# Kernel tuning notes

Hardware: AMD Instinct MI355X
Metric: run time of the kernel (lower is better)

Reference implementation:

```python
import jax, jax.numpy as jnp
import numpy as np
import itertools, math
from collections import Counter

# ----- circuit / state constants -----
M = 12            # modes
NPH = 5           # photons (input_state = [1]*5 + [0]*7)
NTHETA = 12       # trainable phase shifters
NX = 8            # input phase shifters (input_size)
NPARAMS = NTHETA + NX
OUT = 10
TWO_PI = 2.0 * np.pi

# all output Fock states with NPH photons in M modes, as sorted row-index multisets
ROW_IDX = np.array(list(itertools.combinations_with_replacement(range(M), NPH)), np.int32)  # [S, NPH]
S = ROW_IDX.shape[0]  # C(M+NPH-1, NPH) = 4368
# normalization prod(s_j!) for each output state (input state is 0/1 so its factor is 1)
NORM = np.array([np.prod([math.factorial(v) for v in Counter(tuple(r)).values()]) for r in ROW_IDX], np.float32)

# Ryser subsets of the NPH columns
K = 1 << NPH
MASKS = np.array([[(s >> j) & 1 for j in range(NPH)] for s in range(K)], np.float32)  # [K, NPH]
SIGNS = ((-1.0) ** (MASKS.sum(1) + NPH)).astype(np.float32)                            # [K]

# fixed 50/50 beamsplitter layers (perceval BS convention: 1/sqrt2 [[1, i],[i, 1]])
def _bs_layer(pairs):
    Bm = np.eye(M, dtype=np.complex64)
    r = np.float32(1.0 / np.sqrt(2.0))
    for (i, j) in pairs:
        Bm[i, i] = r; Bm[j, j] = r
        Bm[i, j] = 1j * r; Bm[j, i] = 1j * r
    return Bm
BS_EVEN = _bs_layer([(i, i + 1) for i in range(0, M - 1, 2)])
BS_ODD = _bs_layer([(i, i + 1) for i in range(1, M - 1, 2)])


def build_unitaries(x, thetas):
    """x: [B, NX] in [0,1]; thetas: [NTHETA]. Returns batched unitaries [B, M, M] complex64."""
    b = x.shape[0]
    phis = jnp.concatenate([jnp.broadcast_to(thetas, (b, NTHETA)), x * TWO_PI], axis=1)  # [B, NPARAMS]
    U = jnp.broadcast_to(jnp.eye(M, dtype=jnp.complex64), (b, M, M))
    for k in range(NPARAMS):
        mode = k % M
        phase = jnp.exp(1j * phis[:, k])  # [B] complex64
        ph = jnp.ones((b, M), jnp.complex64).at[:, mode].set(phase)
        U = ph[:, :, None] * U                               # apply phase shifter (diag @ U)
        Bm = jnp.asarray(BS_EVEN if k % 2 == 0 else BS_ODD)
        U = jnp.einsum('ij,bjk->bik', Bm, U)                 # apply BS layer
    return U


def slos_distribution(U):
    """Boson-sampling output distribution: p(s) = |perm(U[s_rows, :NPH])|^2 / prod(s_j!)."""
    Ucols = U[:, :, :NPH]  # photons enter modes 0..NPH-1 -> keep those columns, [B, M, NPH]
    masks = jnp.asarray(MASKS).astype(jnp.complex64)
    signs = jnp.asarray(SIGNS).astype(jnp.complex64)
    row_idx = jnp.asarray(ROW_IDX)

    def body(acc, ms):
        mask, sign = ms
        rs = Ucols @ mask              # row sums over subset columns, [B, M]
        rows = rs[:, row_idx]          # gather rows per output state, [B, S, NPH]
        return acc + sign * jnp.prod(rows, axis=-1), None

    acc0 = jnp.zeros((U.shape[0], S), jnp.complex64)
    perm, _ = jax.lax.scan(jax.checkpoint(body), acc0, (masks, signs))  # Ryser over 2^NPH subsets
    probs = (perm.real ** 2 + perm.imag ** 2) / jnp.asarray(NORM)
    return probs  # [B, S]


def setup_inputs() -> dict:
    key = jax.random.key(0)
    k1, k2, k3 = jax.random.split(key, 3)
    x = jax.random.uniform(k1, (512, NX), dtype=jnp.float32)                 # inputs in [0,1]
    thetas = jax.random.uniform(k2, (NTHETA,), dtype=jnp.float32) * np.pi    # init in [0, pi]
    W = jax.random.normal(k3, (S, OUT), dtype=jnp.float32) / np.sqrt(S)      # linear output mapping
    b = jnp.zeros((OUT,), jnp.float32)
    return {"x": x, "thetas": thetas, "W": W, "b": b}


def reference(x, thetas, W, b):
    U = build_unitaries(x, thetas)
    probs = slos_distribution(U)
    return probs @ W + b  # [B, OUT]
```

## Files before the change

### kernel.cpp

```cpp
#include <hip/hip_runtime.h>


#define MODES 12
#define NPH   5
#define KG    16
#define QG    8
#define NPAIR 78
#define S_TOT 4368
#define TPB   512
#define NWAVE (TPB / 64)
#define NOUT  10
#define NPREF 1365

#define TWO_PI_F 6.28318530717958647692f
#define RS2      0.70710678118654752440f

constexpr int Cnk(int n, int r) {
  int p = 1;
  for (int i = 0; i < r; ++i) p = p * (n - i) / (i + 1);
  return p;
}

struct Tables {
  unsigned       pref[NPREF];
  unsigned short cstart[TPB + 1];
  unsigned char  pairs[NPAIR];
};

constexpr Tables make_tables() {
  Tables T{};
  int idx = 0;
  for (int v = 11; v >= 0; --v)
    for (int m0 = 0; m0 <= v; ++m0)
      for (int m1 = m0; m1 <= v; ++m1)
        for (int m2 = m1; m2 <= v; ++m2) {
          int sbase = 0;
          for (int q = 0;  q < m0; ++q) sbase += Cnk(15 - q, 4);
          for (int q = m0; q < m1; ++q) sbase += Cnk(14 - q, 3);
          for (int q = m1; q < m2; ++q) sbase += Cnk(13 - q, 2);
          for (int q = m2; q < v;  ++q) sbase += 12 - q;
          int r1 = 1, pm = 1;
          r1 = (m1 == m0) ? r1 + 1 : 1; pm *= r1;
          r1 = (m2 == m1) ? r1 + 1 : 1; pm *= r1;
          r1 = (v  == m2) ? r1 + 1 : 1; pm *= r1;
          int code = 0;
          if (pm == 1)       code = 0;
          else if (pm == 2)  code = (r1 == 1) ? 1 : 2;
          else if (pm == 4)  code = 3;
          else if (pm == 6)  code = (r1 == 1) ? 4 : 5;
          else               code = 6;
          T.pref[idx++] = ((unsigned)code << 29) | ((unsigned)sbase << 16) |
                          ((unsigned)m0 << 12) | ((unsigned)m1 << 8) |
                          ((unsigned)m2 << 4) | (unsigned)v;
        }
  const long total = 56784;
  long cum = 0;
  int ci = 0;
  T.cstart[0] = 0;
  for (int i = 0; i < NPREF; ++i) {
    int v = (int)(T.pref[i] & 15u);
    cum += 16 + 8 * (12 - v);
    while (ci < TPB - 1 && cum * TPB >= (long)(ci + 1) * total)
      T.cstart[++ci] = (unsigned short)(i + 1);
  }
  while (ci < TPB) T.cstart[++ci] = NPREF;
  int pi = 0;
  for (int a = 0; a < MODES; ++a)
    for (int b = a; b < MODES; ++b)
      T.pairs[pi++] = (unsigned char)((a << 4) | b);
  return T;
}

__constant__ Tables g_tab = make_tables();

__constant__ float2 g_normlut[7] = {
  {1.f / 512.f,   1.f / 256.f},
  {1.f / 1024.f,  1.f / 512.f},
  {1.f / 1536.f,  1.f / 512.f},
  {1.f / 3072.f,  1.f / 1024.f},
  {1.f / 3072.f,  1.f / 1536.f},
  {1.f / 6144.f,  1.f / 1536.f},
  {1.f / 30720.f, 1.f / 6144.f},
};

#define BFLY(i, j)                                                 \
  { float ar = ur[i], ai = ui[i], br = ur[j], bi = ui[j];          \
    ur[i] = RS2 * (ar - bi); ui[i] = RS2 * (ai + br);              \
    ur[j] = RS2 * (br - ai); ui[j] = RS2 * (bi + ar); }

#define PREF(q)                                                     \
  { float4 A = ppt[q][p01], B = ppt[q][p2v];                        \
    pf##q = make_float4(A.x*B.x - A.y*B.y, A.x*B.y + A.y*B.x,       \
                        A.z*B.z - A.w*B.w, A.z*B.w + A.w*B.z); }

#define WSTEP(q, PR, PI)                                            \
  { float4 e2 = rsp[q][w];                                          \
    PR = fmaf(pf##q.x, e2.x, PR); PR = fmaf(-pf##q.y, e2.y, PR);    \
    PI = fmaf(pf##q.x, e2.y, PI); PI = fmaf(pf##q.y, e2.x, PI);     \
    PR = fmaf(pf##q.z, e2.z, PR); PR = fmaf(-pf##q.w, e2.w, PR);    \
    PI = fmaf(pf##q.z, e2.w, PI); PI = fmaf(pf##q.w, e2.z, PI); }

__global__ __launch_bounds__(TPB, 2) void qlayer_kernel(
    const float* __restrict__ x,
    const float* __restrict__ th,
    const float* __restrict__ W,
    const float* __restrict__ bias,
    float* __restrict__ out)
{
  __shared__ float4 rsp[QG][MODES];
  __shared__ float4 ppt[QG][NPAIR];
  __shared__ float  prob_lds[S_TOT];
  __shared__ float2 uc[MODES][NPH];
  __shared__ float2 sc[20];
  __shared__ float  wred[NWAVE][NOUT];

  const int b = blockIdx.x;
  const int t = threadIdx.x;

  if (t < 20) {
    float phi = (t < 12) ? th[t] : x[b * 8 + (t - 12)] * TWO_PI_F;
    float s, c;
    sincosf(phi, &s, &c);
    sc[t] = make_float2(s, c);
  }
  __syncthreads();

  if (t < NPH) {
    float ur[MODES], ui[MODES];
    #pragma unroll
    for (int m = 0; m < MODES; ++m) { ur[m] = 0.f; ui[m] = 0.f; }
    ur[t] = 1.f;
    #pragma unroll
    for (int k = 0; k < 20; ++k) {
      const int mode = k % MODES;
      float sp = sc[k].x, cp = sc[k].y;
      float re = ur[mode] * cp - ui[mode] * sp;
      float im = ur[mode] * sp + ui[mode] * cp;
      ur[mode] = re; ui[mode] = im;
      if ((k & 1) == 0) {
        BFLY(0, 1) BFLY(2, 3) BFLY(4, 5) BFLY(6, 7) BFLY(8, 9) BFLY(10, 11)
      } else {
        BFLY(1, 2) BFLY(3, 4) BFLY(5, 6) BFLY(7, 8) BFLY(9, 10)
      }
    }
    #pragma unroll
    for (int m = 0; m < MODES; ++m) uc[m][t] = make_float2(ur[m], ui[m]);
  }
  __syncthreads();

  if (t < QG * MODES) {
    const int q = t / MODES;
    const int m = t - q * MODES;
    const int k0 = 2 * q, k1 = 2 * q + 1;
    float r0 = uc[m][0].x, i0 = uc[m][0].y;
    float r1 = r0, i1 = i0;
    #pragma unroll
    for (int c = 1; c < NPH; ++c) {
      float ux = uc[m][c].x, uy = uc[m][c].y;
      float d0 = ((k0 >> (c - 1)) & 1) ? -1.f : 1.f;
      float d1 = ((k1 >> (c - 1)) & 1) ? -1.f : 1.f;
      r0 = fmaf(d0, ux, r0); i0 = fmaf(d0, uy, i0);
      r1 = fmaf(d1, ux, r1); i1 = fmaf(d1, uy, i1);
    }
    float sg0 = (__popc((unsigned)k0) & 1) ? -1.f : 1.f;
    float sg1 = (__popc((unsigned)k1) & 1) ? -1.f : 1.f;
    rsp[q][m] = make_float4(sg0 * r0, sg0 * i0, sg1 * r1, sg1 * i1);
  }
  __syncthreads();

  for (int i = t; i < QG * NPAIR; i += TPB) {
    const int q = i / NPAIR;
    const int p = i - q * NPAIR;
    const int ab = (int)g_tab.pairs[p];
    const int a = ab >> 4, b2 = ab & 15;
    float4 A = rsp[q][a], B = rsp[q][b2];
    ppt[q][p] = make_float4(A.x*B.x - A.y*B.y, A.x*B.y + A.y*B.x,
                            A.z*B.z - A.w*B.w, A.z*B.w + A.w*B.z);
  }
  __syncthreads();

  {
    const int beg = g_tab.cstart[t];
    const int end = g_tab.cstart[t + 1];
    for (int j = beg; j < end; ++j) {
      const unsigned e = g_tab.pref[j];
      const int v  = e & 15;
      const int m2 = (e >> 4) & 15;
      const int m1 = (e >> 8) & 15;
      const int m0 = (e >> 12) & 15;
      int si = (int)((e >> 16) & 0x1FFFu);
      const float2 nl = g_normlut[e >> 29];

      const int p01 = (m0 * (25 - m0)) / 2 + (m1 - m0);
      const int p2v = (m2 * (25 - m2)) / 2 + (v  - m2);

      float4 pf0, pf1, pf2, pf3, pf4, pf5, pf6, pf7;
      PREF(0) PREF(1) PREF(2) PREF(3) PREF(4) PREF(5) PREF(6) PREF(7)

      float invn = nl.x;
      for (int w = v; w < MODES; ++w, ++si) {
        float pr0 = 0.f, pi0 = 0.f, pr1 = 0.f, pi1 = 0.f;
        WSTEP(0, pr0, pi0) WSTEP(1, pr0, pi0) WSTEP(2, pr0, pi0) WSTEP(3, pr0, pi0)
        WSTEP(4, pr1, pi1) WSTEP(5, pr1, pi1) WSTEP(6, pr1, pi1) WSTEP(7, pr1, pi1)
        float pr = pr0 + pr1, pi = pi0 + pi1;
        prob_lds[si] = (pr * pr + pi * pi) * invn;
        invn = nl.y;
      }
    }
  }
  __syncthreads();

  float po[NOUT];
  #pragma unroll
  for (int o = 0; o < NOUT; ++o) po[o] = 0.f;

  const float2* __restrict__ W2 = (const float2*)W;
  #pragma unroll 2
  for (int r = 0; r < 8; ++r) {
    const int s = r * TPB + t;
    const float p = prob_lds[s];
    const float2* wr2 = W2 + (size_t)s * 5;
    float2 w01 = wr2[0], w23 = wr2[1], w45 = wr2[2], w67 = wr2[3], w89 = wr2[4];
    po[0] = fmaf(p, w01.x, po[0]); po[1] = fmaf(p, w01.y, po[1]);
    po[2] = fmaf(p, w23.x, po[2]); po[3] = fmaf(p, w23.y, po[3]);
    po[4] = fmaf(p, w45.x, po[4]); po[5] = fmaf(p, w45.y, po[5]);
    po[6] = fmaf(p, w67.x, po[6]); po[7] = fmaf(p, w67.y, po[7]);
    po[8] = fmaf(p, w89.x, po[8]); po[9] = fmaf(p, w89.y, po[9]);
  }
  if (t < S_TOT - 8 * TPB) {
    const int s = 8 * TPB + t;
    const float p = prob_lds[s];
    const float2* wr2 = W2 + (size_t)s * 5;
    float2 w01 = wr2[0], w23 = wr2[1], w45 = wr2[2], w67 = wr2[3], w89 = wr2[4];
    po[0] = fmaf(p, w01.x, po[0]); po[1] = fmaf(p, w01.y, po[1]);
    po[2] = fmaf(p, w23.x, po[2]); po[3] = fmaf(p, w23.y, po[3]);
    po[4] = fmaf(p, w45.x, po[4]); po[5] = fmaf(p, w45.y, po[5]);
    po[6] = fmaf(p, w67.x, po[6]); po[7] = fmaf(p, w67.y, po[7]);
    po[8] = fmaf(p, w89.x, po[8]); po[9] = fmaf(p, w89.y, po[9]);
  }

  #pragma unroll
  for (int o = 0; o < NOUT; ++o) {
    float v = po[o];
    #pragma unroll
    for (int off = 32; off > 0; off >>= 1) v += __shfl_down(v, off, 64);
    po[o] = v;
  }
  const int lane = t & 63, wave = t >> 6;
  if (lane == 0) {
    #pragma unroll
    for (int o = 0; o < NOUT; ++o) wred[wave][o] = po[o];
  }
  __syncthreads();
  if (t < NOUT) {
    float acc = bias[t];
    #pragma unroll
    for (int w2 = 0; w2 < NWAVE; ++w2) acc += wred[w2][t];
    out[b * NOUT + t] = acc;
  }
}

extern "C" void kernel_launch(void* const* d_in, const int* in_sizes, int n_in,
                              void* d_out, int out_size, void* d_ws, size_t ws_size,
                              hipStream_t stream) {
  (void)n_in; (void)out_size; (void)d_ws; (void)ws_size;
  const float* x    = (const float*)d_in[0];
  const float* th   = (const float*)d_in[1];
  const float* W    = (const float*)d_in[2];
  const float* bias = (const float*)d_in[3];
  float* out        = (float*)d_out;
  const int B = in_sizes[0] / 8;
  qlayer_kernel<<<B, TPB, 0, stream>>>(x, th, W, bias, out);
}
```

Measured before the change: 23.89 us.

## Pair two prefixes per work item to share rsp loads in Ryser sum

Each work entry now holds two (m0,m1,m2) prefixes with the same last index v, so every rsp[q][w] value read from LDS feeds two permanent accumulations instead of one. Long rows (v<=4) are split into two half-ranges so per-thread load balancing stays even, and the cstart table is rebuilt from the new per-entry cost. This roughly halves the LDS reads in the hot inner loop and amortises table decode. In exchange it doubles the live prefix registers (16 float4) under a 512x2 launch bound, which risks spills or lower occupancy. Odd-count groups duplicate a prefix, which writes the same value twice.

```diff
diff --git a/kernel.cpp b/kernel.cpp
--- a/kernel.cpp
+++ b/kernel.cpp
@@ -10,7 +10,7 @@
 #define TPB   512
 #define NWAVE (TPB / 64)
 #define NOUT  10
-#define NPREF 1365
+#define NENT  720
 
 #define TWO_PI_F 6.28318530717958647692f
 #define RS2      0.70710678118654752440f
@@ -22,15 +22,19 @@
 }
 
 struct Tables {
-  unsigned       pref[NPREF];
+  unsigned       ea[NENT];
+  unsigned       eb[NENT];
+  unsigned char  wr[NENT];
   unsigned short cstart[TPB + 1];
   unsigned char  pairs[NPAIR];
 };
 
 constexpr Tables make_tables() {
   Tables T{};
-  int idx = 0;
-  for (int v = 11; v >= 0; --v)
+  int ne = 0;
+  for (int v = 11; v >= 0; --v) {
+    unsigned P[364] = {};
+    int cnt = 0;
     for (int m0 = 0; m0 <= v; ++m0)
       for (int m1 = m0; m1 <= v; ++m1)
         for (int m2 = m1; m2 <= v; ++m2) {
@@ -49,21 +53,35 @@
           else if (pm == 4)  code = 3;
           else if (pm == 6)  code = (r1 == 1) ? 4 : 5;
           else               code = 6;
-          T.pref[idx++] = ((unsigned)code << 29) | ((unsigned)sbase << 16) |
-                          ((unsigned)m0 << 12) | ((unsigned)m1 << 8) |
-                          ((unsigned)m2 << 4) | (unsigned)v;
+          P[cnt++] = ((unsigned)code << 29) | ((unsigned)sbase << 16) |
+                     ((unsigned)m0 << 12) | ((unsigned)m1 << 8) |
+                     ((unsigned)m2 << 4) | (unsigned)v;
         }
-  const long total = 56784;
+    const int np = (cnt + 1) / 2;
+    for (int j = 0; j < np; ++j) {
+      unsigned a = P[2 * j];
+      unsigned b = (2 * j + 1 < cnt) ? P[2 * j + 1] : a;
+      if (v <= 4) {
+        int mid = (v + 12) / 2;
+        T.ea[ne] = a; T.eb[ne] = b; T.wr[ne] = (unsigned char)((v << 4) | mid);  ne++;
+        T.ea[ne] = a; T.eb[ne] = b; T.wr[ne] = (unsigned char)((mid << 4) | 12); ne++;
+      } else {
+        T.ea[ne] = a; T.eb[ne] = b; T.wr[ne] = (unsigned char)((v << 4) | 12);   ne++;
+      }
+    }
+  }
+  long total = 0;
+  for (int i = 0; i < NENT; ++i)
+    total += 32 + 8 * ((T.wr[i] & 15) - (T.wr[i] >> 4));
   long cum = 0;
   int ci = 0;
   T.cstart[0] = 0;
-  for (int i = 0; i < NPREF; ++i) {
-    int v = (int)(T.pref[i] & 15u);
-    cum += 16 + 8 * (12 - v);
+  for (int i = 0; i < NENT; ++i) {
+    cum += 32 + 8 * ((T.wr[i] & 15) - (T.wr[i] >> 4));
     while (ci < TPB - 1 && cum * TPB >= (long)(ci + 1) * total)
       T.cstart[++ci] = (unsigned short)(i + 1);
   }
-  while (ci < TPB) T.cstart[++ci] = NPREF;
+  while (ci < TPB) T.cstart[++ci] = NENT;
   int pi = 0;
   for (int a = 0; a < MODES; ++a)
     for (int b = a; b < MODES; ++b)
@@ -88,17 +106,25 @@
     ur[i] = RS2 * (ar - bi); ui[i] = RS2 * (ai + br);              \
     ur[j] = RS2 * (br - ai); ui[j] = RS2 * (bi + ar); }
 
-#define PREF(q)                                                     \
-  { float4 A = ppt[q][p01], B = ppt[q][p2v];                        \
+#define PREFA(q)                                                    \
+  { float4 A = ppt[q][p01a], B = ppt[q][p2va];                      \
     pf##q = make_float4(A.x*B.x - A.y*B.y, A.x*B.y + A.y*B.x,       \
                         A.z*B.z - A.w*B.w, A.z*B.w + A.w*B.z); }
-
-#define WSTEP(q, PR, PI)                                            \
-  { float4 e2 = rsp[q][w];                                          \
-    PR = fmaf(pf##q.x, e2.x, PR); PR = fmaf(-pf##q.y, e2.y, PR);    \
-    PI = fmaf(pf##q.x, e2.y, PI); PI = fmaf(pf##q.y, e2.x, PI);     \
-    PR = fmaf(pf##q.z, e2.z, PR); PR = fmaf(-pf##q.w, e2.w, PR);    \
-    PI = fmaf(pf##q.z, e2.w, PI); PI = fmaf(pf##q.w, e2.z, PI); }
+#define PREFB(q)                                                    \
+  { float4 A = ppt[q][p01b], B = ppt[q][p2vb];                      \
+    pg##q = make_float4(A.x*B.x - A.y*B.y, A.x*B.y + A.y*B.x,       \
+                        A.z*B.z - A.w*B.w, A.z*B.w + A.w*B.z); }
+
+#define WSTEP2(q, PRA, PIA, PRB, PIB)                                   \
+  { float4 e2 = rsp[q][w];                                              \
+    PRA = fmaf(pf##q.x, e2.x, PRA); PRA = fmaf(-pf##q.y, e2.y, PRA);    \
+    PIA = fmaf(pf##q.x, e2.y, PIA); PIA = fmaf(pf##q.y, e2.x, PIA);     \
+    PRA = fmaf(pf##q.z, e2.z, PRA); PRA = fmaf(-pf##q.w, e2.w, PRA);    \
+    PIA = fmaf(pf##q.z, e2.w, PIA); PIA = fmaf(pf##q.w, e2.z, PIA);     \
+    PRB = fmaf(pg##q.x, e2.x, PRB); PRB = fmaf(-pg##q.y, e2.y, PRB);    \
+    PIB = fmaf(pg##q.x, e2.y, PIB); PIB = fmaf(pg##q.y, e2.x, PIB);     \
+    PRB = fmaf(pg##q.z, e2.z, PRB); PRB = fmaf(-pg##q.w, e2.w, PRB);    \
+    PIB = fmaf(pg##q.z, e2.w, PIB); PIB = fmaf(pg##q.w, e2.z, PIB); }
 
 __global__ __launch_bounds__(TPB, 2) void qlayer_kernel(
     const float* __restrict__ x,
@@ -183,28 +209,44 @@
     const int beg = g_tab.cstart[t];
     const int end = g_tab.cstart[t + 1];
     for (int j = beg; j < end; ++j) {
-      const unsigned e = g_tab.pref[j];
-      const int v  = e & 15;
-      const int m2 = (e >> 4) & 15;
-      const int m1 = (e >> 8) & 15;
-      const int m0 = (e >> 12) & 15;
-      int si = (int)((e >> 16) & 0x1FFFu);
-      const float2 nl = g_normlut[e >> 29];
-
-      const int p01 = (m0 * (25 - m0)) / 2 + (m1 - m0);
-      const int p2v = (m2 * (25 - m2)) / 2 + (v  - m2);
+      const unsigned eA = g_tab.ea[j];
+      const unsigned eB = g_tab.eb[j];
+      const int wrj = (int)g_tab.wr[j];
+      const int w0 = wrj >> 4, w1 = wrj & 15;
+
+      const int vA  = eA & 15;
+      const int m2a = (eA >> 4) & 15, m1a = (eA >> 8) & 15, m0a = (eA >> 12) & 15;
+      const int m2b = (eB >> 4) & 15, m1b = (eB >> 8) & 15, m0b = (eB >> 12) & 15;
+      int siA = (int)((eA >> 16) & 0x1FFFu) + (w0 - vA);
+      int siB = (int)((eB >> 16) & 0x1FFFu) + (w0 - vA);
+      const float2 nlA = g_normlut[eA >> 29];
+      const float2 nlB = g_normlut[eB >> 29];
+
+      const int p01a = (m0a * (25 - m0a)) / 2 + (m1a - m0a);
+      const int p2va = (m2a * (25 - m2a)) / 2 + (vA  - m2a);
+      const int p01b = (m0b * (25 - m0b)) / 2 + (m1b - m0b);
+      const int p2vb = (m2b * (25 - m2b)) / 2 + (vA  - m2b);
 
       float4 pf0, pf1, pf2, pf3, pf4, pf5, pf6, pf7;
-      PREF(0) PREF(1) PREF(2) PREF(3) PREF(4) PREF(5) PREF(6) PREF(7)
-
-      float invn = nl.x;
-      for (int w = v; w < MODES; ++w, ++si) {
-        float pr0 = 0.f, pi0 = 0.f, pr1 = 0.f, pi1 = 0.f;
-        WSTEP(0, pr0, pi0) WSTEP(1, pr0, pi0) WSTEP(2, pr0, pi0) WSTEP(3, pr0, pi0)
-        WSTEP(4, pr1, pi1) WSTEP(5, pr1, pi1) WSTEP(6, pr1, pi1) WSTEP(7, pr1, pi1)
-        float pr = pr0 + pr1, pi = pi0 + pi1;
-        prob_lds[si] = (pr * pr + pi * pi) * invn;
-        invn = nl.y;
+      float4 pg0, pg1, pg2, pg3, pg4, pg5, pg6, pg7;
+      PREFA(0) PREFA(1) PREFA(2) PREFA(3) PREFA(4) PREFA(5) PREFA(6) PREFA(7)
+      PREFB(0) PREFB(1) PREFB(2) PREFB(3) PREFB(4) PREFB(5) PREFB(6) PREFB(7)
+
+      float invnA = (w0 == vA) ? nlA.x : nlA.y;
+      float invnB = (w0 == vA) ? nlB.x : nlB.y;
+      for (int w = w0; w < w1; ++w, ++siA, ++siB) {
+        float prA0 = 0.f, piA0 = 0.f, prA1 = 0.f, piA1 = 0.f;
+        float prB0 = 0.f, piB0 = 0.f, prB1 = 0.f, piB1 = 0.f;
+        WSTEP2(0, prA0, piA0, prB0, piB0) WSTEP2(1, prA0, piA0, prB0, piB0)
+        WSTEP2(2, prA0, piA0, prB0, piB0) WSTEP2(3, prA0, piA0, prB0, piB0)
+        WSTEP2(4, prA1, piA1, prB1, piB1) WSTEP2(5, prA1, piA1, prB1, piB1)
+        WSTEP2(6, prA1, piA1, prB1, piB1) WSTEP2(7, prA1, piA1, prB1, piB1)
+        float prA = prA0 + prA1, piA = piA0 + piA1;
+        float prB = prB0 + prB1, piB = piB0 + piB1;
+        prob_lds[siA] = (prA * prA + piA * piA) * invnA;
+        prob_lds[siB] = (prB * prB + piB * piB) * invnB;
+        invnA = nlA.y;
+        invnB = nlB.y;
       }
     }
   }
```

Measured after the change: 23.77 us. Within noise of the previous version (-0.5%).
